# Performance work log

Hardware: AMD Instinct MI355X
Metric: run time of the kernel (lower is better)

The kernel has to match this reference:

```python
import jax, jax.numpy as jnp
import numpy as np

N_GRAPHS = 128  # number of graphs in the batch (max value of `batch`)
NEG_SLOPE = 0.2  # PyG GATConv default LeakyReLU slope


def gat_conv(x, src, dst, W, att_src, att_dst, bias, concat):
    """PyG-style GATConv (eval mode). x: [N, F_in]; src/dst: [E] (self-loops included)."""
    N = x.shape[0]
    H, C = att_src.shape
    xh = (x @ W).reshape(N, H, C)                      # [N, H, C]
    a_src = jnp.sum(xh * att_src, axis=-1)             # [N, H]
    a_dst = jnp.sum(xh * att_dst, axis=-1)             # [N, H]
    alpha = a_src[src] + a_dst[dst]                    # [E, H] edge scores
    alpha = jax.nn.leaky_relu(alpha, NEG_SLOPE)
    # segment softmax over incoming edges of each dst node
    amax = jax.ops.segment_max(alpha, dst, num_segments=N)   # [N, H]
    e = jnp.exp(alpha - amax[dst])                            # [E, H]
    denom = jax.ops.segment_sum(e, dst, num_segments=N)      # [N, H]
    attn = e / denom[dst]                                     # [E, H]
    msg = xh[src] * attn[:, :, None]                          # [E, H, C]
    out = jax.ops.segment_sum(msg, dst, num_segments=N)      # [N, H, C]
    out = out.reshape(N, H * C) if concat else out.mean(axis=1)
    return out + bias


def setup_inputs():
    key = jax.random.key(0)
    ks = jax.random.split(key, 12)
    N, E, F_in, H, C_hid, C_out = 50000, 800000, 128, 8, 32, 10
    x = jax.random.normal(ks[0], (N, F_in), dtype=jnp.float32)
    edge_index = jax.random.randint(ks[1], (2, E), 0, N, dtype=jnp.int32)
    batch = jnp.sort(jax.random.randint(ks[2], (N,), 0, N_GRAPHS, dtype=jnp.int32))
    s_in = 1.0 / np.sqrt(F_in)
    s_h = 1.0 / np.sqrt(H * C_hid)
    W1 = jax.random.normal(ks[3], (F_in, H * C_hid), dtype=jnp.float32) * s_in
    att_src1 = jax.random.normal(ks[4], (H, C_hid), dtype=jnp.float32) * 0.1
    att_dst1 = jax.random.normal(ks[5], (H, C_hid), dtype=jnp.float32) * 0.1
    b1 = jnp.zeros((H * C_hid,), dtype=jnp.float32)
    W2 = jax.random.normal(ks[6], (H * C_hid, C_out), dtype=jnp.float32) * s_h
    att_src2 = jax.random.normal(ks[7], (1, C_out), dtype=jnp.float32) * 0.1
    att_dst2 = jax.random.normal(ks[8], (1, C_out), dtype=jnp.float32) * 0.1
    b2 = jnp.zeros((C_out,), dtype=jnp.float32)
    return {"x": x, "edge_index": edge_index, "batch": batch,
            "W1": W1, "att_src1": att_src1, "att_dst1": att_dst1, "b1": b1,
            "W2": W2, "att_src2": att_src2, "att_dst2": att_dst2, "b2": b2}


def reference(x, edge_index, batch, W1, att_src1, att_dst1, b1, W2, att_src2, att_dst2, b2):
    N = x.shape[0]
    # PyG GATConv default: add self-loops
    loops = jnp.arange(N, dtype=edge_index.dtype)
    src = jnp.concatenate([edge_index[0], loops])
    dst = jnp.concatenate([edge_index[1], loops])
    # eval mode: dropout(p=0.6) is identity
    h = gat_conv(x, src, dst, W1, att_src1, att_dst1, b1, concat=True)   # [N, H*C_hid]
    h = jax.nn.elu(h)
    h = gat_conv(h, src, dst, W2, att_src2, att_dst2, b2, concat=False)  # [N, C_out]
    h = jax.nn.elu(h)
    # global mean pool over graphs
    sums = jax.ops.segment_sum(h, batch, num_segments=N_GRAPHS)          # [G, C_out]
    counts = jax.ops.segment_sum(jnp.ones((N,), h.dtype), batch, num_segments=N_GRAPHS)
    pooled = sums / jnp.maximum(counts, 1.0)[:, None]
    return jax.nn.log_softmax(pooled, axis=1)
```

## Files before the change

### kernel.cpp

```cpp
#include <hip/hip_runtime.h>

#define N_NODES 50000
#define N_EDGES 800000
#define E_TOT   850000
#define F_IN    128
#define HC      256
#define NH      8
#define C_OUT   10
#define N_GRAPH 128
#define NBLK    49
#define XSTRIDE 16
#define NB_DEG  3322

typedef __attribute__((ext_vector_type(8))) short bf16x8;
typedef __attribute__((ext_vector_type(4))) float f32x4;
typedef __attribute__((ext_vector_type(2))) float f32x2;

__device__ __forceinline__ float lrelu(float x){ return x > 0.f ? x : 0.2f * x; }
__device__ __forceinline__ float elu1(float x){ return x > 0.f ? x : (__expf(x) - 1.f); }

__device__ __forceinline__ unsigned short f2bf(float f){
    unsigned int u = __float_as_uint(f);
    return (unsigned short)((u + 0x7fffu + ((u >> 16) & 1u)) >> 16);
}
__device__ __forceinline__ float bf2f(unsigned short h){
    return __uint_as_float((unsigned int)h << 16);
}
__device__ __forceinline__ unsigned char f2fp8(float v){
    unsigned int t = __builtin_amdgcn_cvt_pk_fp8_f32(v, 0.f, 0, false);
    return (unsigned char)(t & 0xffu);
}

__global__ void k_setup(const int* __restrict__ ei, int* __restrict__ deg,
                        const float* __restrict__ W1, unsigned short* __restrict__ bt,
                        const float* __restrict__ W2, float* __restrict__ W2t){
    int b = blockIdx.x;
    if (b < NB_DEG){
        int e = b * 256 + threadIdx.x;
        if (e < E_TOT){
            int dst = (e < N_EDGES) ? ei[N_EDGES + e] : (e - N_EDGES);
            atomicAdd(deg + dst, 1);
        }
    } else if (b < NB_DEG + 128){
        int k = b - NB_DEG;
        int c = threadIdx.x;
        float v = W1[k * HC + c];
        unsigned short hi = f2bf(v);
        unsigned short lo = f2bf(v - bf2f(hi));
        bt[(size_t)c * 256 + k]       = hi;
        bt[(size_t)c * 256 + 128 + k] = lo;
    } else {
        for (int j = threadIdx.x; j < HC * C_OUT; j += 256){
            int k = j / C_OUT, c = j % C_OUT;
            W2t[c * HC + k] = W2[j];
        }
    }
}

__global__ __launch_bounds__(256) void k_gemm1m(const float* __restrict__ x,
                                                const unsigned short* __restrict__ bt,
                                                const float* __restrict__ atts,
                                                const float* __restrict__ attd,
                                                unsigned int* __restrict__ xhb,
                                                float* __restrict__ a_s,
                                                float* __restrict__ a_d){
    __shared__ unsigned char tile[2][32][264];
    __shared__ float sc[2][32][8], dc[2][32][8];
    const int wave = threadIdx.x >> 6, lane = threadIdx.x & 63;
    const int pair = wave >> 1;
    const int h0 = (wave & 1) * 4;
    const int quad = lane >> 4, lidx = lane & 15;
    const int m0 = blockIdx.x * 64 + pair * 32;
    int ar0 = m0 + lidx;      if (ar0 >= N_NODES) ar0 = N_NODES - 1;
    int ar1 = m0 + 16 + lidx; if (ar1 >= N_NODES) ar1 = N_NODES - 1;

    bf16x8 ah0[4], al0[4], ah1[4], al1[4];
    #pragma unroll
    for (int ks = 0; ks < 4; ks++){
        const float* p0 = x + (size_t)ar0 * F_IN + ks * 32 + quad * 8;
        const float* p1 = x + (size_t)ar1 * F_IN + ks * 32 + quad * 8;
        float4 u0 = *(const float4*)p0, u1 = *(const float4*)(p0 + 4);
        float4 w0 = *(const float4*)p1, w1 = *(const float4*)(p1 + 4);
        float v0[8] = {u0.x,u0.y,u0.z,u0.w,u1.x,u1.y,u1.z,u1.w};
        float v1[8] = {w0.x,w0.y,w0.z,w0.w,w1.x,w1.y,w1.z,w1.w};
        bf16x8 h0v, l0v, h1v, l1v;
        #pragma unroll
        for (int j = 0; j < 8; j++){
            unsigned short hh = f2bf(v0[j]);
            h0v[j] = (short)hh;
            l0v[j] = (short)f2bf(v0[j] - bf2f(hh));
            unsigned short hg = f2bf(v1[j]);
            h1v[j] = (short)hg;
            l1v[j] = (short)f2bf(v1[j] - bf2f(hg));
        }
        ah0[ks] = h0v; al0[ks] = l0v; ah1[ks] = h1v; al1[ks] = l1v;
    }

    const uint4* bbase = (const uint4*)bt;
    for (int hh = 0; hh < 4; hh++){
        const int h = h0 + hh;
        float ss0[4] = {0,0,0,0}, ss1[4] = {0,0,0,0};
        float dd0[4] = {0,0,0,0}, dd1[4] = {0,0,0,0};
        #pragma unroll
        for (int sub = 0; sub < 2; sub++){
            int col = h * 32 + sub * 16 + lidx;
            const uint4* bcol = bbase + (size_t)col * 32 + quad;
            bf16x8 bh[4], bl[4];
            #pragma unroll
            for (int ks = 0; ks < 4; ks++){
                bh[ks] = __builtin_bit_cast(bf16x8, bcol[ks * 4]);
                bl[ks] = __builtin_bit_cast(bf16x8, bcol[16 + ks * 4]);
            }
            f32x4 a0A = {0.f,0.f,0.f,0.f}, a0B = {0.f,0.f,0.f,0.f}, a0C = {0.f,0.f,0.f,0.f};
            f32x4 a1A = {0.f,0.f,0.f,0.f}, a1B = {0.f,0.f,0.f,0.f}, a1C = {0.f,0.f,0.f,0.f};
            #pragma unroll
            for (int ks = 0; ks < 4; ks++){
                a0A = __builtin_amdgcn_mfma_f32_16x16x32_bf16(ah0[ks], bh[ks], a0A, 0, 0, 0);
                a1A = __builtin_amdgcn_mfma_f32_16x16x32_bf16(ah1[ks], bh[ks], a1A, 0, 0, 0);
                a0B = __builtin_amdgcn_mfma_f32_16x16x32_bf16(ah0[ks], bl[ks], a0B, 0, 0, 0);
                a1B = __builtin_amdgcn_mfma_f32_16x16x32_bf16(ah1[ks], bl[ks], a1B, 0, 0, 0);
                a0C = __builtin_amdgcn_mfma_f32_16x16x32_bf16(al0[ks], bh[ks], a0C, 0, 0, 0);
                a1C = __builtin_amdgcn_mfma_f32_16x16x32_bf16(al1[ks], bh[ks], a1C, 0, 0, 0);
            }
            f32x4 acc0, acc1;
            #pragma unroll
            for (int reg = 0; reg < 4; reg++){
                acc0[reg] = (a0A[reg] + a0B[reg]) + a0C[reg];
                acc1[reg] = (a1A[reg] + a1B[reg]) + a1C[reg];
            }
            float sv = atts[col], dv = attd[col];
            #pragma unroll
            for (int reg = 0; reg < 4; reg++){
                tile[pair][quad*4+reg][col]    = f2fp8(acc0[reg]);
                tile[pair][16+quad*4+reg][col] = f2fp8(acc1[reg]);
                ss0[reg] += acc0[reg] * sv;  dd0[reg] += acc0[reg] * dv;
                ss1[reg] += acc1[reg] * sv;  dd1[reg] += acc1[reg] * dv;
            }
        }
        #pragma unroll
        for (int reg = 0; reg < 4; reg++){
            float a = ss0[reg], b = dd0[reg], c = ss1[reg], d = dd1[reg];
            a += __shfl_xor(a,1,64); a += __shfl_xor(a,2,64); a += __shfl_xor(a,4,64); a += __shfl_xor(a,8,64);
            b += __shfl_xor(b,1,64); b += __shfl_xor(b,2,64); b += __shfl_xor(b,4,64); b += __shfl_xor(b,8,64);
            c += __shfl_xor(c,1,64); c += __shfl_xor(c,2,64); c += __shfl_xor(c,4,64); c += __shfl_xor(c,8,64);
            d += __shfl_xor(d,1,64); d += __shfl_xor(d,2,64); d += __shfl_xor(d,4,64); d += __shfl_xor(d,8,64);
            if (lidx == 0){
                sc[pair][quad*4+reg][h]    = a;  dc[pair][quad*4+reg][h]    = b;
                sc[pair][16+quad*4+reg][h] = c;  dc[pair][16+quad*4+reg][h] = d;
            }
        }
    }
    __syncthreads();
    const int rbase = (wave & 1) * 16;
    for (int r = 0; r < 16; r++){
        int row = m0 + rbase + r;
        if (row < N_NODES){
            unsigned int p = *(const unsigned int*)&tile[pair][rbase + r][lane * 4];
            xhb[(size_t)row * 64 + lane] = p;
        }
    }
    {
        int linear = lane * 2;
        int row = m0 + rbase + (linear >> 3);
        if (row < N_NODES){
            const float* sb = &sc[pair][rbase][0];
            const float* db = &dc[pair][rbase][0];
            float2 s2 = *(const float2*)(sb + linear);
            float2 d2 = *(const float2*)(db + linear);
            *(float2*)(a_s + (size_t)row * NH + (linear & 7)) = s2;
            *(float2*)(a_d + (size_t)row * NH + (linear & 7)) = d2;
        }
    }
}

__global__ void k_bsum(const int* __restrict__ deg, int* __restrict__ bsum, int* __restrict__ rowp){
    int b = blockIdx.x;
    int v = 0;
    for (int i = threadIdx.x; i < 1024; i += 256){
        int idx = b * 1024 + i;
        if (idx < N_NODES) v += deg[idx];
    }
    #pragma unroll
    for (int off = 1; off < 64; off <<= 1) v += __shfl_xor(v, off, 64);
    __shared__ int sd[4];
    if ((threadIdx.x & 63) == 0) sd[threadIdx.x >> 6] = v;
    __syncthreads();
    if (threadIdx.x == 0){
        bsum[b] = sd[0] + sd[1] + sd[2] + sd[3];
        if (b == 0) rowp[N_NODES] = E_TOT;
    }
}

__global__ __launch_bounds__(1024) void k_scan(const int* __restrict__ deg, const int* __restrict__ bsum,
                                               int* __restrict__ rowp, int* __restrict__ cur){
    __shared__ int sd[1024];
    int b = blockIdx.x;
    int bex = 0;
    for (int j = 0; j < b; j++) bex += bsum[j];
    int i = b * 1024 + threadIdx.x;
    int v = (i < N_NODES) ? deg[i] : 0;
    sd[threadIdx.x] = v;
    __syncthreads();
    for (int off = 1; off < 1024; off <<= 1){
        int t = (threadIdx.x >= off) ? sd[threadIdx.x - off] : 0;
        __syncthreads();
        sd[threadIdx.x] += t;
        __syncthreads();
    }
    if (i < N_NODES){
        int excl = sd[threadIdx.x] - v + bex;
        rowp[i] = excl;
        cur[i]  = excl;
    }
}

__global__ void k_scatter(const int* __restrict__ ei, int* __restrict__ cur, int* __restrict__ col){
    int e = blockIdx.x * 256 + threadIdx.x;
    if (e >= E_TOT) return;
    int s, d;
    if (e < N_EDGES){ s = ei[e]; d = ei[N_EDGES + e]; }
    else { s = e - N_EDGES; d = s; }
    int slot = atomicAdd(cur + d, 1);
    col[slot] = s;
}

__global__ __launch_bounds__(256) void k_agg1f(const unsigned int* __restrict__ xhb,
                                               const float* __restrict__ a_s, const float* __restrict__ a_d,
                                               const int* __restrict__ rowp, const int* __restrict__ colb,
                                               const float* __restrict__ b1, const float* __restrict__ W2t,
                                               const float* __restrict__ as2, const float* __restrict__ ad2,
                                               float* __restrict__ xh2){
    int wave = threadIdx.x >> 6, lane = threadIdx.x & 63;
    int half = lane >> 5, l32 = lane & 31;
    int n = blockIdx.x * 8 + wave * 2 + half;
    int h = l32 >> 2;
    float adh = a_d[(unsigned)(n * NH + h)];
    int s0 = rowp[n], s1 = rowp[n + 1];
    const uint2* xv = (const uint2*)xhb;
    f32x2 a01 = {0.f,0.f}, a23 = {0.f,0.f}, a45 = {0.f,0.f}, a67 = {0.f,0.f};
    float den = 0.f;
    int idx = s0;
    for (; idx + 3 < s1; idx += 4){
        int sA = colb[idx], sB = colb[idx+1], sC = colb[idx+2], sD = colb[idx+3];
        float eA = a_s[(unsigned)(sA * NH + h)];
        float eB = a_s[(unsigned)(sB * NH + h)];
        float eC = a_s[(unsigned)(sC * NH + h)];
        float eD = a_s[(unsigned)(sD * NH + h)];
        uint2 pA = xv[(unsigned)(sA * 32 + l32)];
        uint2 pB = xv[(unsigned)(sB * 32 + l32)];
        uint2 pC = xv[(unsigned)(sC * 32 + l32)];
        uint2 pD = xv[(unsigned)(sD * 32 + l32)];
        float wA = __expf(lrelu(eA + adh));
        float wB = __expf(lrelu(eB + adh));
        float wC = __expf(lrelu(eC + adh));
        float wD = __expf(lrelu(eD + adh));
        den += (wA + wB) + (wC + wD);
        f32x2 w2;
        w2[0] = wA; w2[1] = wA;
        a01 += w2 * __builtin_amdgcn_cvt_pk_f32_fp8(pA.x, false);
        a23 += w2 * __builtin_amdgcn_cvt_pk_f32_fp8(pA.x, true);
        a45 += w2 * __builtin_amdgcn_cvt_pk_f32_fp8(pA.y, false);
        a67 += w2 * __builtin_amdgcn_cvt_pk_f32_fp8(pA.y, true);
        w2[0] = wB; w2[1] = wB;
        a01 += w2 * __builtin_amdgcn_cvt_pk_f32_fp8(pB.x, false);
        a23 += w2 * __builtin_amdgcn_cvt_pk_f32_fp8(pB.x, true);
        a45 += w2 * __builtin_amdgcn_cvt_pk_f32_fp8(pB.y, false);
        a67 += w2 * __builtin_amdgcn_cvt_pk_f32_fp8(pB.y, true);
        w2[0] = wC; w2[1] = wC;
        a01 += w2 * __builtin_amdgcn_cvt_pk_f32_fp8(pC.x, false);
        a23 += w2 * __builtin_amdgcn_cvt_pk_f32_fp8(pC.x, true);
        a45 += w2 * __builtin_amdgcn_cvt_pk_f32_fp8(pC.y, false);
        a67 += w2 * __builtin_amdgcn_cvt_pk_f32_fp8(pC.y, true);
        w2[0] = wD; w2[1] = wD;
        a01 += w2 * __builtin_amdgcn_cvt_pk_f32_fp8(pD.x, false);
        a23 += w2 * __builtin_amdgcn_cvt_pk_f32_fp8(pD.x, true);
        a45 += w2 * __builtin_amdgcn_cvt_pk_f32_fp8(pD.y, false);
        a67 += w2 * __builtin_amdgcn_cvt_pk_f32_fp8(pD.y, true);
    }
    for (; idx < s1; idx++){
        int sA = colb[idx];
        float wA = __expf(lrelu(a_s[(unsigned)(sA * NH + h)] + adh));
        den += wA;
        uint2 pA = xv[(unsigned)(sA * 32 + l32)];
        f32x2 w2; w2[0] = wA; w2[1] = wA;
        a01 += w2 * __builtin_amdgcn_cvt_pk_f32_fp8(pA.x, false);
        a23 += w2 * __builtin_amdgcn_cvt_pk_f32_fp8(pA.x, true);
        a45 += w2 * __builtin_amdgcn_cvt_pk_f32_fp8(pA.y, false);
        a67 += w2 * __builtin_amdgcn_cvt_pk_f32_fp8(pA.y, true);
    }
    float rden = 1.f / den;
    const float4* b4 = (const float4*)b1;
    float4 bb0 = b4[l32 * 2], bb1 = b4[l32 * 2 + 1];
    float r0 = elu1(a01[0] * rden + bb0.x);
    float r1 = elu1(a01[1] * rden + bb0.y);
    float r2 = elu1(a23[0] * rden + bb0.z);
    float r3 = elu1(a23[1] * rden + bb0.w);
    float r4 = elu1(a45[0] * rden + bb1.x);
    float r5 = elu1(a45[1] * rden + bb1.y);
    float r6 = elu1(a67[0] * rden + bb1.z);
    float r7 = elu1(a67[1] * rden + bb1.w);
    float o[C_OUT];
    #pragma unroll
    for (int c = 0; c < C_OUT; c++){
        const float4* w4 = (const float4*)(W2t + c * HC);
        float4 w0 = w4[l32 * 2], w1 = w4[l32 * 2 + 1];
        float v = r0*w0.x + r1*w0.y + r2*w0.z + r3*w0.w
                + r4*w1.x + r5*w1.y + r6*w1.z + r7*w1.w;
        v += __shfl_xor(v, 1, 64); v += __shfl_xor(v, 2, 64); v += __shfl_xor(v, 4, 64);
        v += __shfl_xor(v, 8, 64); v += __shfl_xor(v, 16, 64);
        o[c] = v;
    }
    if (l32 == 0){
        float s2 = 0.f, d2 = 0.f;
        #pragma unroll
        for (int c = 0; c < C_OUT; c++){ s2 += o[c] * as2[c]; d2 += o[c] * ad2[c]; }
        float* xr = xh2 + (unsigned)(n * XSTRIDE);
        *(float4*)(xr)     = make_float4(o[0], o[1], o[2], o[3]);
        *(float4*)(xr + 4) = make_float4(o[4], o[5], o[6], o[7]);
        *(float4*)(xr + 8) = make_float4(o[8], o[9], s2, d2);
    }
}

__global__ __launch_bounds__(256) void k_agg2(const float* __restrict__ xh2,
                                              const int* __restrict__ rowp, const int* __restrict__ colb,
                                              const float* __restrict__ b2,
                                              float* __restrict__ h2){
    int grp = threadIdx.x >> 4, l16 = threadIdx.x & 15;
    int n = blockIdx.x * 16 + grp;
    if (n >= N_NODES) return;
    float adn = xh2[(unsigned)(n * XSTRIDE + 11)];
    int s0 = rowp[n], s1 = rowp[n + 1];
    float acc[C_OUT] = {};
    float den = 0.f;
    for (int idx = s0 + l16; idx < s1; idx += 16){
        int s = colb[idx];
        const float* xr = xh2 + (unsigned)(s * XSTRIDE);
        float4 q0 = *(const float4*)(xr);
        float4 q1 = *(const float4*)(xr + 4);
        float4 q2 = *(const float4*)(xr + 8);
        float w = __expf(lrelu(q2.z + adn));
        den += w;
        acc[0] += w*q0.x; acc[1] += w*q0.y; acc[2] += w*q0.z; acc[3] += w*q0.w;
        acc[4] += w*q1.x; acc[5] += w*q1.y; acc[6] += w*q1.z; acc[7] += w*q1.w;
        acc[8] += w*q2.x; acc[9] += w*q2.y;
    }
    #pragma unroll
    for (int off = 1; off < 16; off <<= 1){
        den += __shfl_xor(den, off, 64);
        #pragma unroll
        for (int c = 0; c < C_OUT; c++) acc[c] += __shfl_xor(acc[c], off, 64);
    }
    if (l16 == 0){
        float rden = 1.f / den;
        #pragma unroll
        for (int c = 0; c < C_OUT; c++)
            h2[(unsigned)(n * C_OUT + c)] = elu1(acc[c] * rden + b2[c]);
    }
}

__global__ __launch_bounds__(256) void k_pool(const float* __restrict__ h2, const int* __restrict__ batch,
                                              float* __restrict__ out){
    int g = blockIdx.x;
    int l = 0, r = N_NODES;
    while (l < r){ int m = (l + r) >> 1; if (batch[m] < g) l = m + 1; else r = m; }
    int lo = l;
    l = 0; r = N_NODES;
    while (l < r){ int m = (l + r) >> 1; if (batch[m] < g + 1) l = m + 1; else r = m; }
    int hi = l;
    float acc[C_OUT] = {};
    for (int i = lo + (int)threadIdx.x; i < hi; i += 256){
        const float* row = h2 + (size_t)i * C_OUT;
        #pragma unroll
        for (int c = 0; c < C_OUT; c++) acc[c] += row[c];
    }
    #pragma unroll
    for (int c = 0; c < C_OUT; c++){
        #pragma unroll
        for (int off = 32; off > 0; off >>= 1) acc[c] += __shfl_xor(acc[c], off, 64);
    }
    __shared__ float sd[4][C_OUT];
    int wave = threadIdx.x >> 6, lane = threadIdx.x & 63;
    if (lane == 0){
        #pragma unroll
        for (int c = 0; c < C_OUT; c++) sd[wave][c] = acc[c];
    }
    __syncthreads();
    if (threadIdx.x == 0){
        float cnt = (float)(hi - lo);
        if (cnt < 1.f) cnt = 1.f;
        float v[C_OUT];
        float m = -1e30f;
        #pragma unroll
        for (int c = 0; c < C_OUT; c++){
            v[c] = (sd[0][c] + sd[1][c] + sd[2][c] + sd[3][c]) / cnt;
            m = fmaxf(m, v[c]);
        }
        float sum = 0.f;
        #pragma unroll
        for (int c = 0; c < C_OUT; c++) sum += __expf(v[c] - m);
        float lse = m + __logf(sum);
        #pragma unroll
        for (int c = 0; c < C_OUT; c++) out[g * C_OUT + c] = v[c] - lse;
    }
}

extern "C" void kernel_launch(void* const* d_in, const int* in_sizes, int n_in,
                              void* d_out, int out_size, void* d_ws, size_t ws_size,
                              hipStream_t stream){
    const float* x    = (const float*)d_in[0];
    const int*   ei   = (const int*)d_in[1];
    const int*   batch= (const int*)d_in[2];
    const float* W1   = (const float*)d_in[3];
    const float* as1  = (const float*)d_in[4];
    const float* ad1  = (const float*)d_in[5];
    const float* b1   = (const float*)d_in[6];
    const float* W2   = (const float*)d_in[7];
    const float* as2v = (const float*)d_in[8];
    const float* ad2v = (const float*)d_in[9];
    const float* b2   = (const float*)d_in[10];
    float* out = (float*)d_out;

    char* ws = (char*)d_ws;
    size_t off = 0;
    auto alloc = [&](size_t bytes)->char*{
        char* p = ws + off;
        off = (off + bytes + 255) & ~(size_t)255;
        return p;
    };
    unsigned int* xhb  = (unsigned int*)alloc((size_t)N_NODES * HC);
    unsigned short* bt = (unsigned short*)alloc((size_t)HC * 256 * 2);
    float* asc1 = (float*)alloc((size_t)N_NODES * NH * 4);
    float* adc1 = (float*)alloc((size_t)N_NODES * NH * 4);
    int*   deg  = (int*)alloc((size_t)N_NODES * 4);
    int*   rowp = (int*)alloc((size_t)(N_NODES + 1) * 4);
    int*   cur  = (int*)alloc((size_t)N_NODES * 4);
    int*   colb = (int*)alloc((size_t)E_TOT * 4);
    int*   bsum = (int*)alloc(64 * 4);
    float* xh2  = (float*)alloc((size_t)N_NODES * XSTRIDE * 4);
    float* W2t  = (float*)alloc((size_t)HC * C_OUT * 4);
    float* h2   = (float*)alloc((size_t)N_NODES * C_OUT * 4);
    (void)ws_size; (void)in_sizes; (void)n_in; (void)out_size;

    hipMemsetAsync(deg, 0, (size_t)N_NODES * 4, stream);
    hipLaunchKernelGGL(k_setup,   dim3(NB_DEG + 129), dim3(256), 0, stream, ei, deg, W1, bt, W2, W2t);
    hipLaunchKernelGGL(k_gemm1m,  dim3(782),   dim3(256), 0, stream, x, bt, as1, ad1, xhb, asc1, adc1);
    hipLaunchKernelGGL(k_bsum,    dim3(NBLK),  dim3(256), 0, stream, deg, bsum, rowp);
    hipLaunchKernelGGL(k_scan,    dim3(NBLK),  dim3(1024),0, stream, deg, bsum, rowp, cur);
    hipLaunchKernelGGL(k_scatter, dim3((E_TOT + 255)/256), dim3(256), 0, stream, ei, cur, colb);
    hipLaunchKernelGGL(k_agg1f,   dim3(N_NODES / 8), dim3(256), 0, stream, xhb, asc1, adc1, rowp, colb, b1, W2t, as2v, ad2v, xh2);
    hipLaunchKernelGGL(k_agg2,    dim3((N_NODES + 15)/16), dim3(256), 0, stream, xh2, rowp, colb, b2, h2);
    hipLaunchKernelGGL(k_pool,    dim3(N_GRAPH), dim3(256), 0, stream, h2, batch, out);
}
```

Before: 300.7 us.

## Give each GEMM wave all heads with prefetched B, and store edge sources as 16-bit

The layer-1 GEMM kernel now has each wave compute 32 rows across all 8 heads, so a block covers 128 rows and the grid is halved. The next column tile's B fragments are loaded into registers while the current MFMAs run, and the a_s/a_d outputs are written as float4. Separately, the CSR source-index array is stored as unsigned short instead of int, which halves index traffic in scatter and both aggregation kernels. The 16-bit indices only work while the node count stays below 65536. Fewer, larger GEMM blocks can balance worse across CUs, and the extra prefetch registers may lower occupancy.

```diff
diff --git a/kernel.cpp b/kernel.cpp
--- a/kernel.cpp
+++ b/kernel.cpp
@@ -64,13 +64,11 @@
                                                 unsigned int* __restrict__ xhb,
                                                 float* __restrict__ a_s,
                                                 float* __restrict__ a_d){
-    __shared__ unsigned char tile[2][32][264];
-    __shared__ float sc[2][32][8], dc[2][32][8];
+    __shared__ unsigned char tile[4][32][264];
+    __shared__ float sc[4][32][8], dc[4][32][8];
     const int wave = threadIdx.x >> 6, lane = threadIdx.x & 63;
-    const int pair = wave >> 1;
-    const int h0 = (wave & 1) * 4;
     const int quad = lane >> 4, lidx = lane & 15;
-    const int m0 = blockIdx.x * 64 + pair * 32;
+    const int m0 = blockIdx.x * 128 + wave * 32;
     int ar0 = m0 + lidx;      if (ar0 >= N_NODES) ar0 = N_NODES - 1;
     int ar1 = m0 + 16 + lidx; if (ar1 >= N_NODES) ar1 = N_NODES - 1;
 
@@ -97,19 +95,31 @@
     }
 
     const uint4* bbase = (const uint4*)bt;
-    for (int hh = 0; hh < 4; hh++){
-        const int h = h0 + hh;
+    bf16x8 bh[4], bl[4];
+    {
+        const uint4* bcol = bbase + (size_t)lidx * 32 + quad;
+        #pragma unroll
+        for (int ks = 0; ks < 4; ks++){
+            bh[ks] = __builtin_bit_cast(bf16x8, bcol[ks * 4]);
+            bl[ks] = __builtin_bit_cast(bf16x8, bcol[16 + ks * 4]);
+        }
+    }
+    for (int h = 0; h < NH; h++){
         float ss0[4] = {0,0,0,0}, ss1[4] = {0,0,0,0};
         float dd0[4] = {0,0,0,0}, dd1[4] = {0,0,0,0};
         #pragma unroll
         for (int sub = 0; sub < 2; sub++){
             int col = h * 32 + sub * 16 + lidx;
-            const uint4* bcol = bbase + (size_t)col * 32 + quad;
-            bf16x8 bh[4], bl[4];
-            #pragma unroll
-            for (int ks = 0; ks < 4; ks++){
-                bh[ks] = __builtin_bit_cast(bf16x8, bcol[ks * 4]);
-                bl[ks] = __builtin_bit_cast(bf16x8, bcol[16 + ks * 4]);
+            bf16x8 nh[4], nl[4];
+            int tn = h * 2 + sub + 1;
+            if (tn < 16){
+                int ncol = (tn >> 1) * 32 + (tn & 1) * 16 + lidx;
+                const uint4* nb = bbase + (size_t)ncol * 32 + quad;
+                #pragma unroll
+                for (int ks = 0; ks < 4; ks++){
+                    nh[ks] = __builtin_bit_cast(bf16x8, nb[ks * 4]);
+                    nl[ks] = __builtin_bit_cast(bf16x8, nb[16 + ks * 4]);
+                }
             }
             f32x4 a0A = {0.f,0.f,0.f,0.f}, a0B = {0.f,0.f,0.f,0.f}, a0C = {0.f,0.f,0.f,0.f};
             f32x4 a1A = {0.f,0.f,0.f,0.f}, a1B = {0.f,0.f,0.f,0.f}, a1C = {0.f,0.f,0.f,0.f};
@@ -131,11 +141,13 @@
             float sv = atts[col], dv = attd[col];
             #pragma unroll
             for (int reg = 0; reg < 4; reg++){
-                tile[pair][quad*4+reg][col]    = f2fp8(acc0[reg]);
-                tile[pair][16+quad*4+reg][col] = f2fp8(acc1[reg]);
+                tile[wave][quad*4+reg][col]    = f2fp8(acc0[reg]);
+                tile[wave][16+quad*4+reg][col] = f2fp8(acc1[reg]);
                 ss0[reg] += acc0[reg] * sv;  dd0[reg] += acc0[reg] * dv;
                 ss1[reg] += acc1[reg] * sv;  dd1[reg] += acc1[reg] * dv;
             }
+            #pragma unroll
+            for (int ks = 0; ks < 4; ks++){ bh[ks] = nh[ks]; bl[ks] = nl[ks]; }
         }
         #pragma unroll
         for (int reg = 0; reg < 4; reg++){
@@ -145,30 +157,29 @@
             c += __shfl_xor(c,1,64); c += __shfl_xor(c,2,64); c += __shfl_xor(c,4,64); c += __shfl_xor(c,8,64);
             d += __shfl_xor(d,1,64); d += __shfl_xor(d,2,64); d += __shfl_xor(d,4,64); d += __shfl_xor(d,8,64);
             if (lidx == 0){
-                sc[pair][quad*4+reg][h]    = a;  dc[pair][quad*4+reg][h]    = b;
-                sc[pair][16+quad*4+reg][h] = c;  dc[pair][16+quad*4+reg][h] = d;
+                sc[wave][quad*4+reg][h]    = a;  dc[wave][quad*4+reg][h]    = b;
+                sc[wave][16+quad*4+reg][h] = c;  dc[wave][16+quad*4+reg][h] = d;
             }
         }
     }
     __syncthreads();
-    const int rbase = (wave & 1) * 16;
-    for (int r = 0; r < 16; r++){
-        int row = m0 + rbase + r;
+    for (int r = 0; r < 32; r++){
+        int row = m0 + r;
         if (row < N_NODES){
-            unsigned int p = *(const unsigned int*)&tile[pair][rbase + r][lane * 4];
+            unsigned int p = *(const unsigned int*)&tile[wave][r][lane * 4];
             xhb[(size_t)row * 64 + lane] = p;
         }
     }
     {
-        int linear = lane * 2;
-        int row = m0 + rbase + (linear >> 3);
+        int linear = lane * 4;
+        int row = m0 + (linear >> 3);
         if (row < N_NODES){
-            const float* sb = &sc[pair][rbase][0];
-            const float* db = &dc[pair][rbase][0];
-            float2 s2 = *(const float2*)(sb + linear);
-            float2 d2 = *(const float2*)(db + linear);
-            *(float2*)(a_s + (size_t)row * NH + (linear & 7)) = s2;
-            *(float2*)(a_d + (size_t)row * NH + (linear & 7)) = d2;
+            const float* sb = &sc[wave][0][0];
+            const float* db = &dc[wave][0][0];
+            float4 s4 = *(const float4*)(sb + linear);
+            float4 d4 = *(const float4*)(db + linear);
+            *(float4*)(a_s + (size_t)m0 * NH + linear) = s4;
+            *(float4*)(a_d + (size_t)m0 * NH + linear) = d4;
         }
     }
 }
@@ -214,19 +225,20 @@
     }
 }
 
-__global__ void k_scatter(const int* __restrict__ ei, int* __restrict__ cur, int* __restrict__ col){
+__global__ void k_scatter(const int* __restrict__ ei, int* __restrict__ cur,
+                          unsigned short* __restrict__ col){
     int e = blockIdx.x * 256 + threadIdx.x;
     if (e >= E_TOT) return;
     int s, d;
     if (e < N_EDGES){ s = ei[e]; d = ei[N_EDGES + e]; }
     else { s = e - N_EDGES; d = s; }
     int slot = atomicAdd(cur + d, 1);
-    col[slot] = s;
+    col[slot] = (unsigned short)s;
 }
 
 __global__ __launch_bounds__(256) void k_agg1f(const unsigned int* __restrict__ xhb,
                                                const float* __restrict__ a_s, const float* __restrict__ a_d,
-                                               const int* __restrict__ rowp, const int* __restrict__ colb,
+                                               const int* __restrict__ rowp, const unsigned short* __restrict__ colb,
                                                const float* __restrict__ b1, const float* __restrict__ W2t,
                                                const float* __restrict__ as2, const float* __restrict__ ad2,
                                                float* __restrict__ xh2){
@@ -322,7 +334,7 @@
 }
 
 __global__ __launch_bounds__(256) void k_agg2(const float* __restrict__ xh2,
-                                              const int* __restrict__ rowp, const int* __restrict__ colb,
+                                              const int* __restrict__ rowp, const unsigned short* __restrict__ colb,
                                               const float* __restrict__ b2,
                                               float* __restrict__ h2){
     int grp = threadIdx.x >> 4, l16 = threadIdx.x & 15;
@@ -434,7 +446,7 @@
     int*   deg  = (int*)alloc((size_t)N_NODES * 4);
     int*   rowp = (int*)alloc((size_t)(N_NODES + 1) * 4);
     int*   cur  = (int*)alloc((size_t)N_NODES * 4);
-    int*   colb = (int*)alloc((size_t)E_TOT * 4);
+    unsigned short* colb = (unsigned short*)alloc((size_t)E_TOT * 2);
     int*   bsum = (int*)alloc(64 * 4);
     float* xh2  = (float*)alloc((size_t)N_NODES * XSTRIDE * 4);
     float* W2t  = (float*)alloc((size_t)HC * C_OUT * 4);
@@ -443,7 +455,7 @@
 
     hipMemsetAsync(deg, 0, (size_t)N_NODES * 4, stream);
     hipLaunchKernelGGL(k_setup,   dim3(NB_DEG + 129), dim3(256), 0, stream, ei, deg, W1, bt, W2, W2t);
-    hipLaunchKernelGGL(k_gemm1m,  dim3(782),   dim3(256), 0, stream, x, bt, as1, ad1, xhb, asc1, adc1);
+    hipLaunchKernelGGL(k_gemm1m,  dim3(391),   dim3(256), 0, stream, x, bt, as1, ad1, xhb, asc1, adc1);
     hipLaunchKernelGGL(k_bsum,    dim3(NBLK),  dim3(256), 0, stream, deg, bsum, rowp);
     hipLaunchKernelGGL(k_scan,    dim3(NBLK),  dim3(1024),0, stream, deg, bsum, rowp, cur);
     hipLaunchKernelGGL(k_scatter, dim3((E_TOT + 255)/256), dim3(256), 0, stream, ei, cur, colb);
```

After: 282.8 us. 5.9% less time.
